# Kernel optimization log

Measured on AMD Instinct MI355X. Metric: run time of the kernel, lower is better.

## Reference

```python
import jax, jax.numpy as jnp
import numpy as np

N_PARTIAL = 1024  # matches init_kwargs


def setup_inputs() -> dict:
    key = jax.random.key(0)
    k1, k2 = jax.random.split(key)
    B, H, L = 8, 768, 4096
    x = jax.random.normal(k1, (B, H, L), dtype=jnp.float32)
    k = jax.random.normal(k2, (H, L), dtype=jnp.float32)
    return {"x": x, "k": k}


def reference(x, k):
    # FFT-based causal long convolution with low-pass frequency truncation.
    L = x.shape[-1]
    N = 2 * L  # zero-pad to 2L for linear (non-circular) convolution
    x_dtype = x.dtype
    x_f = jnp.fft.rfft(x.astype(jnp.float32), n=N)          # [B, H, N//2+1] complex64
    k_f = jnp.fft.rfft(k.astype(jnp.float32), n=N)          # [H, N//2+1]   complex64
    # zero out all frequency bins >= N_partial // 2 (low-pass truncation of the kernel)
    freqs = jnp.arange(N // 2 + 1)
    k_f = jnp.where(freqs < N_PARTIAL // 2, k_f, jnp.zeros((), dtype=k_f.dtype))
    y_f = x_f * k_f                                          # broadcast over batch
    y = jnp.fft.irfft(y_f, n=N)[..., :L].astype(x_dtype)     # [B, H, L]
    return y
```

## Files before the change

### kernel.cpp

```cpp
#include <hip/hip_runtime.h>
#include <math.h>

#define LSEQ 4096
#define NFFT 8192
#define NF   512
#define NF2  1024
#define NH   768
#define NBH  6144
#define MROWS 6912
#define SPLIT_ROW 3584

typedef __attribute__((ext_vector_type(8))) short short8;
typedef __attribute__((ext_vector_type(4))) float floatx4;

__device__ __forceinline__ unsigned short f2bf(float f) {
    unsigned int u = __float_as_uint(f);
    u += 0x7fff + ((u >> 16) & 1);
    return (unsigned short)(u >> 16);
}

__device__ __forceinline__ void gld16(const unsigned short* g, const unsigned short* l) {
    __builtin_amdgcn_global_load_lds(
        (const __attribute__((address_space(1))) void*)g,
        (__attribute__((address_space(3))) void*)l, 16, 0, 0);
}

__global__ void build_tables(unsigned short* __restrict__ T1,
                             unsigned short* __restrict__ T2) {
    __shared__ unsigned short tile[64][66];
    const int t = threadIdx.x;
    const int F0 = blockIdx.x * 64;
    const int N0 = blockIdx.y * 64;
#pragma unroll
    for (int i = 0; i < 16; ++i) {
        int r = (t >> 6) + i * 4;
        int c = t & 63;
        int f2 = F0 + r, n = N0 + c;
        int f = f2 >> 1;
        int p = (f * n) & (NFFT - 1);
        float th = (float)p * (float)(2.0 * M_PI / (double)NFFT);
        float s, cc;
        sincosf(th, &s, &cc);
        unsigned short v = f2bf((f2 & 1) ? s : cc);
        T1[(size_t)f2 * LSEQ + n] = v;
        tile[r][c] = v;
    }
    __syncthreads();
#pragma unroll
    for (int i = 0; i < 16; ++i) {
        int r = (t >> 6) + i * 4;
        int c = t & 63;
        T2[(size_t)(N0 + r) * NF2 + F0 + c] = tile[c][r];
    }
}

__global__ void tobf16(const float* __restrict__ x, const float* __restrict__ kk,
                       unsigned short* __restrict__ o) {
    size_t e = ((size_t)blockIdx.x * 256 + threadIdx.x) * 4;
    const size_t XN = (size_t)NBH * LSEQ;
    const float* s = (e < XN) ? (x + e) : (kk + (e - XN));
    float4 v = *(const float4*)s;
    unsigned int lo = (unsigned int)f2bf(v.x) | ((unsigned int)f2bf(v.y) << 16);
    unsigned int hi = (unsigned int)f2bf(v.z) | ((unsigned int)f2bf(v.w) << 16);
    *(uint2*)(o + e) = make_uint2(lo, hi);
}

__global__ __launch_bounds__(512) void gemm8(
    const unsigned short* __restrict__ A,
    const unsigned short* __restrict__ B,
    float* __restrict__ C,
    float* __restrict__ P1a,
    float* __restrict__ P1b,
    int gx, int gy, int N, int ldk, int Ksub)
{
    __shared__ __align__(16) unsigned short S[2 * 32768];
    const int t = threadIdx.x;
    const int wid = t >> 6, l = t & 63;

    const int nwg = gridDim.x, bid = blockIdx.x;
    const int swz = (bid & 7) * (nwg >> 3) + (bid >> 3);
    const int bx = swz % gx;
    const int rem = swz / gx;
    const int by = rem % gy;
    const int bz = rem / gy;

    const int m0 = by * 256, n0 = bx * 256;
    const int wr = wid >> 2, wc = wid & 3;
    const int lq = l >> 4, lr = l & 15;
    const int kbase = bz * Ksub;
    const int NT = Ksub >> 6;

    const int sx = ((lr >> 2) & 1) << 1;
    const int s0 = lq ^ sx;
    const int aoff = (wr * 128 + lr) * 64 + s0 * 8;
    const int boff = 16384 + (wc * 64 + lr) * 64 + s0 * 8;

    const int gsl = (l & 7) ^ (((l >> 5) & 1) << 1);
    const unsigned short* pAs = A + (size_t)(m0 + wid * 8 + (l >> 3)) * ldk + kbase + gsl * 8;
    const unsigned short* pBs = B + (size_t)(n0 + wid * 8 + (l >> 3)) * ldk + kbase + gsl * 8;

    floatx4 acc[8][4];
#pragma unroll
    for (int i = 0; i < 8; ++i)
#pragma unroll
        for (int j = 0; j < 4; ++j)
            acc[i][j] = (floatx4){0.f, 0.f, 0.f, 0.f};

#define STG_A(b, h, kt_)                                                                  \
    gld16(pAs + (size_t)((h)*128     ) * ldk + (kt_) * 64, S + (b)*32768 +         ((h)*128      + wid*8) * 64); \
    gld16(pAs + (size_t)((h)*128 + 64) * ldk + (kt_) * 64, S + (b)*32768 +         ((h)*128 + 64 + wid*8) * 64);
#define STG_B(b, h, kt_)                                                                  \
    gld16(pBs + (size_t)((h)*128     ) * ldk + (kt_) * 64, S + (b)*32768 + 16384 + ((h)*128      + wid*8) * 64); \
    gld16(pBs + (size_t)((h)*128 + 64) * ldk + (kt_) * 64, S + (b)*32768 + 16384 + ((h)*128 + 64 + wid*8) * 64);

#define RD_A(Sc, ip)                                                           \
    _Pragma("unroll") for (int ii = 0; ii < 2; ++ii)                           \
    _Pragma("unroll") for (int ks = 0; ks < 2; ++ks)                           \
        aq[ii][ks] = *(const short8*)((Sc) + aoff + 1024 * ((ip) + ii) + 32 * ks);
#define RD_B(Sc)                                                               \
    _Pragma("unroll") for (int j = 0; j < 4; ++j)                              \
    _Pragma("unroll") for (int ks = 0; ks < 2; ++ks)                           \
        bq[j][ks] = *(const short8*)((Sc) + boff + 1024 * j + 32 * ks);
#define MM(ip)                                                                 \
    __builtin_amdgcn_s_setprio(1);                                             \
    _Pragma("unroll") for (int ii = 0; ii < 2; ++ii)                           \
    _Pragma("unroll") for (int j = 0; j < 4; ++j)                              \
    _Pragma("unroll") for (int ks = 0; ks < 2; ++ks)                           \
        acc[(ip) + ii][j] = __builtin_amdgcn_mfma_f32_16x16x32_bf16(           \
            aq[ii][ks], bq[j][ks], acc[(ip) + ii][j], 0, 0, 0);                \
    __builtin_amdgcn_s_setprio(0);

    STG_A(0, 0, 0) STG_A(0, 1, 0) STG_B(0, 0, 0) STG_B(0, 1, 0)
    asm volatile("s_waitcnt vmcnt(0)" ::: "memory");
    __builtin_amdgcn_s_barrier();

    short8 aq[2][2], bq[4][2];

    for (int kt = 0; kt < NT; ++kt) {
        const unsigned short* Sc = S + (size_t)(kt & 1) * 32768;
        const int bs = (kt & 1) ^ 1;
        const bool pf = (kt + 1 < NT);
        if (pf) { STG_A(bs, 0, kt + 1) }
        if (pf) asm volatile("s_waitcnt vmcnt(2)" ::: "memory");
        else    asm volatile("s_waitcnt vmcnt(0)" ::: "memory");
        __builtin_amdgcn_s_barrier();
        RD_B(Sc) RD_A(Sc, 0)
        MM(0)
        __builtin_amdgcn_s_barrier();
        if (pf) { STG_A(bs, 1, kt + 1) }
        RD_A(Sc, 2)
        __builtin_amdgcn_s_barrier();
        MM(2)
        __builtin_amdgcn_s_barrier();
        if (pf) { STG_B(bs, 0, kt + 1) }
        RD_A(Sc, 4)
        __builtin_amdgcn_s_barrier();
        MM(4)
        __builtin_amdgcn_s_barrier();
        if (pf) { STG_B(bs, 1, kt + 1) }
        RD_A(Sc, 6)
        __builtin_amdgcn_s_barrier();
        MM(6)
        __builtin_amdgcn_s_barrier();
    }

    float* Cb;
    if (bz == 0) Cb = C;
    else Cb = (m0 < SPLIT_ROW) ? P1a : (P1b - (size_t)SPLIT_ROW * N);
#pragma unroll
    for (int i = 0; i < 8; ++i)
#pragma unroll
        for (int j = 0; j < 4; ++j)
#pragma unroll
            for (int r = 0; r < 4; ++r) {
                int row = m0 + wr * 128 + 16 * i + lq * 4 + r;
                int col = n0 + wc * 64 + 16 * j + lr;
                Cb[(size_t)row * N + col] = acc[i][j][r];
            }
}

__global__ void combine(const float* __restrict__ C1,
                        const float* __restrict__ P1a,
                        const float* __restrict__ P1b,
                        unsigned short* __restrict__ AB) {
    int idx = blockIdx.x * blockDim.x + threadIdx.x;
    int bh = idx >> 9;
    int f = idx & (NF - 1);
    int h = bh % NH;
    const float* xc = C1 + (size_t)bh * NF2 + 2 * f;
    const float* xp = (bh < SPLIT_ROW)
        ? (P1a + (size_t)bh * NF2 + 2 * f)
        : (P1b + (size_t)(bh - SPLIT_ROW) * NF2 + 2 * f);
    const int kr = NBH + h;
    const float* kc = C1 + (size_t)kr * NF2 + 2 * f;
    const float* kp = P1b + (size_t)(kr - SPLIT_ROW) * NF2 + 2 * f;
    float Xre = xc[0] + xp[0], Xim = -(xc[1] + xp[1]);
    float Kre = kc[0] + kp[0], Kim = -(kc[1] + kp[1]);
    float s = (f == 0 ? 1.0f : 2.0f) * (1.0f / (float)NFFT);
    float Av = s * (Xre * Kre - Xim * Kim);
    float Bv = -(s * (Xre * Kim + Xim * Kre));
    unsigned int packed = (unsigned int)f2bf(Av) | ((unsigned int)f2bf(Bv) << 16);
    *(unsigned int*)(AB + (size_t)bh * NF2 + 2 * f) = packed;
}

extern "C" void kernel_launch(void* const* d_in, const int* in_sizes, int n_in,
                              void* d_out, int out_size, void* d_ws, size_t ws_size,
                              hipStream_t stream) {
    const float* x = (const float*)d_in[0];
    const float* k = (const float*)d_in[1];
    float* y = (float*)d_out;

    unsigned short* T1 = (unsigned short*)d_ws;
    unsigned short* T2 = T1 + (size_t)NF2 * LSEQ;
    unsigned short* AB = T2 + (size_t)LSEQ * NF2;
    float* P1a = (float*)(AB + (size_t)NBH * NF2);

    unsigned short* Abm = (unsigned short*)d_out;
    float* C1 = (float*)((char*)d_out + (size_t)MROWS * LSEQ * 2);
    float* P1b = C1 + (size_t)MROWS * NF2;

    const int blk = 256;
    hipLaunchKernelGGL(build_tables, dim3(NF2 / 64, LSEQ / 64), dim3(blk), 0, stream, T1, T2);
    hipLaunchKernelGGL(tobf16, dim3((MROWS * LSEQ / 4) / blk), dim3(blk), 0, stream, x, k, Abm);
    hipLaunchKernelGGL(gemm8, dim3(4 * 27 * 2), dim3(512), 0, stream,
                       Abm, T1, C1, P1a, P1b, 4, 27, NF2, LSEQ, LSEQ / 2);
    hipLaunchKernelGGL(combine, dim3((NBH * NF) / blk), dim3(blk), 0, stream, C1, P1a, P1b, AB);
    hipLaunchKernelGGL(gemm8, dim3(16 * 24), dim3(512), 0, stream,
                       AB, T2, y, (float*)nullptr, (float*)nullptr, 16, 24, LSEQ, NF2, NF2);
}
```

Before: 331.5 us.

## Prefetch whole K-tile upfront, drop intra-tile barriers, use full 8-way LDS swizzle

The bf16 MFMA GEMM main loop now issues all eight global-to-LDS loads for the next K tile at the start of each iteration. It then runs the four LDS-read and MFMA phases back to back, with a single wait and barrier at the end, replacing the old interleaved stage/barrier sequence of about eight barriers per tile. The LDS swizzle becomes a full 8-way XOR on row mod 8, matched on the write and read side, to cut bank conflicts on the ds_reads. The aim is fewer barrier stalls and less LDS contention. The cost is more outstanding loads at once and less fine-grained overlap between loading and compute.

Measured after the change: 309.7 us. -6.6%, faster.

```diff
diff --git a/kernel.cpp b/kernel.cpp
--- a/kernel.cpp
+++ b/kernel.cpp
@@ -90,12 +90,11 @@
     const int kbase = bz * Ksub;
     const int NT = Ksub >> 6;
 
-    const int sx = ((lr >> 2) & 1) << 1;
-    const int s0 = lq ^ sx;
+    const int s0 = lq ^ (lr & 7);
     const int aoff = (wr * 128 + lr) * 64 + s0 * 8;
     const int boff = 16384 + (wc * 64 + lr) * 64 + s0 * 8;
 
-    const int gsl = (l & 7) ^ (((l >> 5) & 1) << 1);
+    const int gsl = (l & 7) ^ ((l >> 3) & 7);
     const unsigned short* pAs = A + (size_t)(m0 + wid * 8 + (l >> 3)) * ldk + kbase + gsl * 8;
     const unsigned short* pBs = B + (size_t)(n0 + wid * 8 + (l >> 3)) * ldk + kbase + gsl * 8;
 
@@ -106,21 +105,24 @@
         for (int j = 0; j < 4; ++j)
             acc[i][j] = (floatx4){0.f, 0.f, 0.f, 0.f};
 
-#define STG_A(b, h, kt_)                                                                  \
-    gld16(pAs + (size_t)((h)*128     ) * ldk + (kt_) * 64, S + (b)*32768 +         ((h)*128      + wid*8) * 64); \
-    gld16(pAs + (size_t)((h)*128 + 64) * ldk + (kt_) * 64, S + (b)*32768 +         ((h)*128 + 64 + wid*8) * 64);
-#define STG_B(b, h, kt_)                                                                  \
-    gld16(pBs + (size_t)((h)*128     ) * ldk + (kt_) * 64, S + (b)*32768 + 16384 + ((h)*128      + wid*8) * 64); \
-    gld16(pBs + (size_t)((h)*128 + 64) * ldk + (kt_) * 64, S + (b)*32768 + 16384 + ((h)*128 + 64 + wid*8) * 64);
+#define STG_TILE(b, kt_)                                                                   \
+    gld16(pAs + (size_t)  0 * ldk + (kt_) * 64, S + (b)*32768 +         (  0 + wid*8) * 64); \
+    gld16(pAs + (size_t) 64 * ldk + (kt_) * 64, S + (b)*32768 +         ( 64 + wid*8) * 64); \
+    gld16(pAs + (size_t)128 * ldk + (kt_) * 64, S + (b)*32768 +         (128 + wid*8) * 64); \
+    gld16(pAs + (size_t)192 * ldk + (kt_) * 64, S + (b)*32768 +         (192 + wid*8) * 64); \
+    gld16(pBs + (size_t)  0 * ldk + (kt_) * 64, S + (b)*32768 + 16384 + (  0 + wid*8) * 64); \
+    gld16(pBs + (size_t) 64 * ldk + (kt_) * 64, S + (b)*32768 + 16384 + ( 64 + wid*8) * 64); \
+    gld16(pBs + (size_t)128 * ldk + (kt_) * 64, S + (b)*32768 + 16384 + (128 + wid*8) * 64); \
+    gld16(pBs + (size_t)192 * ldk + (kt_) * 64, S + (b)*32768 + 16384 + (192 + wid*8) * 64);
 
 #define RD_A(Sc, ip)                                                           \
     _Pragma("unroll") for (int ii = 0; ii < 2; ++ii)                           \
     _Pragma("unroll") for (int ks = 0; ks < 2; ++ks)                           \
-        aq[ii][ks] = *(const short8*)((Sc) + aoff + 1024 * ((ip) + ii) + 32 * ks);
+        aq[ii][ks] = *(const short8*)((Sc) + ((aoff ^ (ks * 32)) + 1024 * ((ip) + ii)));
 #define RD_B(Sc)                                                               \
     _Pragma("unroll") for (int j = 0; j < 4; ++j)                              \
     _Pragma("unroll") for (int ks = 0; ks < 2; ++ks)                           \
-        bq[j][ks] = *(const short8*)((Sc) + boff + 1024 * j + 32 * ks);
+        bq[j][ks] = *(const short8*)((Sc) + ((boff ^ (ks * 32)) + 1024 * j));
 #define MM(ip)                                                                 \
     __builtin_amdgcn_s_setprio(1);                                             \
     _Pragma("unroll") for (int ii = 0; ii < 2; ++ii)                           \
@@ -130,9 +132,10 @@
             aq[ii][ks], bq[j][ks], acc[(ip) + ii][j], 0, 0, 0);                \
     __builtin_amdgcn_s_setprio(0);
 
-    STG_A(0, 0, 0) STG_A(0, 1, 0) STG_B(0, 0, 0) STG_B(0, 1, 0)
+    STG_TILE(0, 0)
     asm volatile("s_waitcnt vmcnt(0)" ::: "memory");
     __builtin_amdgcn_s_barrier();
+    __builtin_amdgcn_sched_barrier(0);
 
     short8 aq[2][2], bq[4][2];
 
@@ -140,28 +143,17 @@
         const unsigned short* Sc = S + (size_t)(kt & 1) * 32768;
         const int bs = (kt & 1) ^ 1;
         const bool pf = (kt + 1 < NT);
-        if (pf) { STG_A(bs, 0, kt + 1) }
-        if (pf) asm volatile("s_waitcnt vmcnt(2)" ::: "memory");
-        else    asm volatile("s_waitcnt vmcnt(0)" ::: "memory");
-        __builtin_amdgcn_s_barrier();
-        RD_B(Sc) RD_A(Sc, 0)
-        MM(0)
-        __builtin_amdgcn_s_barrier();
-        if (pf) { STG_A(bs, 1, kt + 1) }
-        RD_A(Sc, 2)
-        __builtin_amdgcn_s_barrier();
-        MM(2)
-        __builtin_amdgcn_s_barrier();
-        if (pf) { STG_B(bs, 0, kt + 1) }
-        RD_A(Sc, 4)
-        __builtin_amdgcn_s_barrier();
-        MM(4)
-        __builtin_amdgcn_s_barrier();
-        if (pf) { STG_B(bs, 1, kt + 1) }
-        RD_A(Sc, 6)
-        __builtin_amdgcn_s_barrier();
-        MM(6)
-        __builtin_amdgcn_s_barrier();
+        if (pf) { STG_TILE(bs, kt + 1) }
+        RD_B(Sc)
+        RD_A(Sc, 0) MM(0)
+        RD_A(Sc, 2) MM(2)
+        RD_A(Sc, 4) MM(4)
+        RD_A(Sc, 6) MM(6)
+        if (pf) {
+            asm volatile("s_waitcnt vmcnt(0)" ::: "memory");
+            __builtin_amdgcn_s_barrier();
+            __builtin_amdgcn_sched_barrier(0);
+        }
     }
 
     float* Cb;
```
